# Kernel tuning notes

Hardware: AMD Instinct MI355X
Metric: run time of the kernel (lower is better)

The kernel has to match this reference:

```python
import jax, jax.numpy as jnp
import numpy as np

B, S, E, H = 8, 2048, 1024, 4
D = E // H  # per-head attention embed_dim (torch MHA with num_heads=1)


def setup_inputs() -> dict:
    key = jax.random.key(0)
    ks = jax.random.split(key, 7)
    scale = 0.02
    return {
        "x": jax.random.normal(ks[0], (B, S, E), dtype=jnp.float32),
        # outer linear: torch Linear(E, E) -> y = x @ W.T + b
        "W_lin": jax.random.normal(ks[1], (E, E), dtype=jnp.float32) * scale,
        "b_lin": jnp.zeros((E,), dtype=jnp.float32),
        # per-head MultiheadAttention params, stacked over H heads
        # in_proj: [3D, D] weight, [3D] bias per head (q,k,v stacked)
        "W_in": jax.random.normal(ks[2], (H, 3 * D, D), dtype=jnp.float32) * scale,
        "b_in": jnp.zeros((H, 3 * D), dtype=jnp.float32),
        # out_proj: [D, D] weight, [D] bias per head
        "W_out": jax.random.normal(ks[3], (H, D, D), dtype=jnp.float32) * scale,
        "b_out": jnp.zeros((H, D), dtype=jnp.float32),
    }


def _forward(x, W_lin, b_lin, W_in, b_in, W_out, b_out):
    # outer projection
    x_proj = jnp.einsum("bse,fe->bsf", x, W_lin) + b_lin          # [B,S,E]
    # torch.chunk(dim=-1) into H contiguous slices of width D == reshape
    xs = x_proj.reshape(B, S, H, D)                                 # [B,S,H,D]
    # per-head in_proj (q,k,v share input; weights stacked as [3D, D])
    qkv = jnp.einsum("bshd,hed->bshe", xs, W_in) + b_in             # [B,S,H,3D]
    q, k, v = jnp.split(qkv, 3, axis=-1)                            # each [B,S,H,D]
    # scaled dot-product attention per head (inner num_heads=1 -> head dim D)
    scores = jnp.einsum("bshd,bthd->bhst", q, k) / jnp.sqrt(jnp.float32(D))
    attn = jax.nn.softmax(scores, axis=-1)                          # [B,H,S,S]
    out = jnp.einsum("bhst,bthd->bshd", attn, v)                    # [B,S,H,D]
    # per-head out_proj
    out = jnp.einsum("bshd,hed->bshe", out, W_out) + b_out          # [B,S,H,D]
    # concat heads back along feature dim
    return out.reshape(B, S, E)


def reference(x, W_lin, b_lin, W_in, b_in, W_out, b_out):
    return _forward(x, W_lin, b_lin, W_in, b_in, W_out, b_out)
```

## Files before the change

kernel.cpp:

```cpp
#include <hip/hip_runtime.h>


typedef unsigned short u16;
typedef short s8v __attribute__((ext_vector_type(8)));
typedef float f4v __attribute__((ext_vector_type(4)));
typedef unsigned short us8v __attribute__((ext_vector_type(8)));

typedef const __attribute__((address_space(1))) void* gas_t;
typedef __attribute__((address_space(3))) void* las_t;

#define QSCALE 0.09016844f

__device__ __forceinline__ u16 f2bf(float f) {
  unsigned u = __builtin_bit_cast(unsigned, f);
  unsigned r = u + 0x7FFFu + ((u >> 16) & 1u);
  return (u16)(r >> 16);
}

__device__ __forceinline__ unsigned cvtpk(float a, float b) {
  unsigned r;
  asm("v_cvt_pk_bf16_f32 %0, %1, %2" : "=v"(r) : "v"(a), "v"(b));
  return r;
}

__device__ __forceinline__ void gload16(const void* g, void* l) {
  __builtin_amdgcn_global_load_lds((gas_t)g, (las_t)l, 16, 0, 0);
}

__global__ void cast_kernel(const float* __restrict__ in, u16* __restrict__ out, int n4) {
  int i = blockIdx.x * blockDim.x + threadIdx.x;
  const int stride = gridDim.x * blockDim.x;
  for (; i < n4; i += stride) {
    const float4 v = reinterpret_cast<const float4*>(in)[i];
    ushort4 o;
    o.x = f2bf(v.x); o.y = f2bf(v.y); o.z = f2bf(v.z); o.w = f2bf(v.w);
    reinterpret_cast<ushort4*>(out)[i] = o;
  }
}

__global__ void cast_win(const float* __restrict__ in, u16* __restrict__ out, int n4) {
  const int i = blockIdx.x * blockDim.x + threadIdx.x;
  if (i >= n4) return;
  const float4 v = reinterpret_cast<const float4*>(in)[i];
  const float sc = (((i >> 6) % 768) < 256) ? QSCALE : 1.0f;
  ushort4 o;
  o.x = f2bf(v.x * sc); o.y = f2bf(v.y * sc); o.z = f2bf(v.z * sc); o.w = f2bf(v.w * sc);
  reinterpret_cast<ushort4*>(out)[i] = o;
}

template <int MODE>
__global__ void __launch_bounds__(256, 2) gemm128(
    const u16* __restrict__ A, const u16* __restrict__ Bw,
    const float* __restrict__ bias,
    u16* __restrict__ outB, float* __restrict__ outF,
    u16* __restrict__ Qo, u16* __restrict__ Ko, u16* __restrict__ Vo)
{
  constexpr int K    = (MODE == 0) ? 1024 : 256;
  constexpr int LDA  = 1024;
  constexpr int LDB  = (MODE == 0) ? 1024 : 256;
  constexpr int SMEM = (MODE == 1) ? 35072 : 32768;

  const int bx = blockIdx.x, ny = blockIdx.y, h = blockIdx.z;
  const int tid = threadIdx.x;
  const int wid = tid >> 6, l = tid & 63;
  const int l15 = l & 15, lg = l >> 4;
  const int wr = wid >> 1, wc = wid & 1;

  __shared__ __align__(16) char smem[SMEM];
  char* Al = smem;
  char* Bl = smem + 16384;

  const u16* Abase = A + (size_t)bx * 128 * LDA + ((MODE == 0) ? 0 : h * 256);
  const size_t bwoff = (MODE == 0) ? 0
                      : ((MODE == 1) ? (size_t)h * 768 * 256 : (size_t)h * 256 * 256);
  const u16* Bbase = Bw + bwoff + (size_t)ny * 128 * LDB;

  f4v acc[4][4];
#pragma unroll
  for (int i = 0; i < 4; ++i)
#pragma unroll
    for (int j = 0; j < 4; ++j) acc[i][j] = f4v{0.f, 0.f, 0.f, 0.f};

  for (int k0 = 0; k0 < K; k0 += 64) {
    __syncthreads();
#pragma unroll
    for (int ii = 0; ii < 4; ++ii) {
      const int i = wid * 4 + ii;
      const int row = i * 8 + (l >> 3);
      const int c = l & 7;
      gload16(Abase + (size_t)row * LDA + k0 + ((c ^ (row & 7)) << 3), Al + i * 1024);
    }
#pragma unroll
    for (int ii = 0; ii < 4; ++ii) {
      const int i = wid * 4 + ii;
      const int row = i * 8 + (l >> 3);
      const int c = l & 7;
      gload16(Bbase + (size_t)row * LDB + k0 + ((c ^ (row & 7)) << 3), Bl + i * 1024);
    }
    __syncthreads();
#pragma unroll
    for (int kf = 0; kf < 2; ++kf) {
      s8v a[4];
#pragma unroll
      for (int mf = 0; mf < 4; ++mf) {
        const int row = wr * 64 + mf * 16 + l15;
        a[mf] = *reinterpret_cast<const s8v*>(
            Al + row * 128 + (((kf * 32 + lg * 8) << 1) ^ ((row & 7) << 4)));
      }
#pragma unroll
      for (int nf = 0; nf < 4; ++nf) {
        const int n = wc * 64 + nf * 16 + l15;
        const s8v b = *reinterpret_cast<const s8v*>(
            Bl + n * 128 + (((kf * 32 + lg * 8) << 1) ^ ((n & 7) << 4)));
#pragma unroll
        for (int mf = 0; mf < 4; ++mf)
          acc[mf][nf] = __builtin_amdgcn_mfma_f32_16x16x32_bf16(a[mf], b, acc[mf][nf], 0, 0, 0);
      }
    }
  }

  const int mbase = bx * 128 + wr * 64;
  const int nbase = ny * 128 + wc * 64;

  if constexpr (MODE == 0) {
#pragma unroll
    for (int nf = 0; nf < 4; ++nf) {
      const int colg = nbase + nf * 16 + l15;
      const float bv = bias[colg];
#pragma unroll
      for (int mf = 0; mf < 4; ++mf)
#pragma unroll
        for (int r = 0; r < 4; ++r) {
          const int mr = mbase + mf * 16 + lg * 4 + r;
          outB[(size_t)mr * 1024 + colg] = f2bf(acc[mf][nf][r] + bv);
        }
    }
  } else if constexpr (MODE == 2) {
#pragma unroll
    for (int nf = 0; nf < 4; ++nf) {
      const int colg = nbase + nf * 16 + l15;
      const float bv = bias[h * 256 + colg];
#pragma unroll
      for (int mf = 0; mf < 4; ++mf)
#pragma unroll
        for (int r = 0; r < 4; ++r) {
          const int mr = mbase + mf * 16 + lg * 4 + r;
          outF[(size_t)mr * 1024 + h * 256 + colg] = acc[mf][nf][r] + bv;
        }
    }
  } else {
    if (ny < 4) {
      u16* dst = (ny < 2) ? Qo : Ko;
      const int cb = (ny < 2) ? 0 : 256;
      const float bscale = (ny < 2) ? QSCALE : 1.0f;
#pragma unroll
      for (int nf = 0; nf < 4; ++nf) {
        const int colg = nbase + nf * 16 + l15;
        const float bv = bias[h * 768 + colg] * bscale;
        const int d = colg - cb;
#pragma unroll
        for (int mf = 0; mf < 4; ++mf)
#pragma unroll
          for (int r = 0; r < 4; ++r) {
            const int mr = mbase + mf * 16 + lg * 4 + r;
            const int b = mr >> 11, s = mr & 2047;
            dst[((size_t)(b * 4 + h) * 2048 + s) * 256 + d] = f2bf(acc[mf][nf][r] + bv);
          }
      }
    } else {
      __syncthreads();
      short* tr = reinterpret_cast<short*>(smem);
#pragma unroll
      for (int nf = 0; nf < 4; ++nf) {
        const int colg = nbase + nf * 16 + l15;
        const float bv = bias[h * 768 + colg];
        const int cl = wc * 64 + nf * 16 + l15;
#pragma unroll
        for (int mf = 0; mf < 4; ++mf)
#pragma unroll
          for (int r = 0; r < 4; ++r) {
            const int rl = wr * 64 + mf * 16 + lg * 4 + r;
            tr[rl * 137 + cl] = (short)f2bf(acc[mf][nf][r] + bv);
          }
      }
      __syncthreads();
      const int b = bx >> 4;
#pragma unroll
      for (int rep = 0; rep < 8; ++rep) {
        const int u = rep * 256 + tid;
        const int d = u >> 4, sb = u & 15;
        const int dglob = (ny - 4) * 128 + d;
        const int tile = (bx & 15) * 2 + (sb >> 3);
        const int c = sb & 7;
        const int kA = 32 * (c >> 2) + 8 * ((2 * c) & 3) + 4 * ((c >> 1) & 1);
        u16* base = Vo + (((size_t)(b * 4 + h) * 32 + tile) * 256 + dglob) * 64;
        ushort4 lo, hi;
        lo.x = (u16)tr[(sb * 8 + 0) * 137 + d];
        lo.y = (u16)tr[(sb * 8 + 1) * 137 + d];
        lo.z = (u16)tr[(sb * 8 + 2) * 137 + d];
        lo.w = (u16)tr[(sb * 8 + 3) * 137 + d];
        hi.x = (u16)tr[(sb * 8 + 4) * 137 + d];
        hi.y = (u16)tr[(sb * 8 + 5) * 137 + d];
        hi.z = (u16)tr[(sb * 8 + 6) * 137 + d];
        hi.w = (u16)tr[(sb * 8 + 7) * 137 + d];
        *reinterpret_cast<ushort4*>(base + kA)     = lo;
        *reinterpret_cast<ushort4*>(base + kA + 8) = hi;
      }
    }
  }
}

__global__ void __launch_bounds__(256, 2) attn_fwd(
    const u16* __restrict__ Q, const u16* __restrict__ Kk,
    const u16* __restrict__ Vt, u16* __restrict__ AO)
{
  const int qt = blockIdx.x;
  const int bh = blockIdx.y;
  const int tid = threadIdx.x;
  const int wid = tid >> 6, l = tid & 63;
  const int l15 = l & 15, lg = l >> 4;

  __shared__ __align__(16) char smem[65536];
  char* Kl = smem;
  char* Vl = smem + 32768;

  const size_t kbase = (size_t)bh * 2048 * 256;

  s8v qa[8];
  {
    const u16* qrow = Q + ((size_t)bh * 2048 + qt * 64 + wid * 16 + l15) * 256;
#pragma unroll
    for (int kf = 0; kf < 8; ++kf)
      qa[kf] = *reinterpret_cast<const s8v*>(qrow + kf * 32 + lg * 8);
  }

  f4v O[16];
#pragma unroll
  for (int df = 0; df < 16; ++df) O[df] = f4v{0.f, 0.f, 0.f, 0.f};
  float m_run = -1e30f, l_run = 0.f;

  for (int t0 = 0; t0 < 2048; t0 += 64) {
    __syncthreads();
#pragma unroll
    for (int ii = 0; ii < 8; ++ii) {
      const int i = wid * 8 + ii;
      const int row = i * 2 + (l >> 5);
      const int c = l & 31;
      gload16(Kk + kbase + (size_t)(t0 + row) * 256 + ((c ^ (row & 7)) << 3), Kl + i * 1024);
    }
    {
      const u16* vtile = Vt + ((size_t)bh * 32 + (t0 >> 6)) * 16384;
#pragma unroll
      for (int ii = 0; ii < 8; ++ii) {
        const int i = wid * 8 + ii;
        const int d = i * 8 + (l >> 3);
        const int c = l & 7;
        gload16(vtile + (size_t)d * 64 + ((c ^ (d & 7)) << 3), Vl + i * 1024);
      }
    }
    __syncthreads();

    f4v Sx[4];
#pragma unroll
    for (int nf = 0; nf < 4; ++nf) Sx[nf] = f4v{0.f, 0.f, 0.f, 0.f};
#pragma unroll
    for (int kf = 0; kf < 8; ++kf) {
      const int ch = kf * 4 + lg;
#pragma unroll
      for (int nf = 0; nf < 4; ++nf) {
        const int tl = nf * 16 + l15;
        const s8v kb = *reinterpret_cast<const s8v*>(
            Kl + tl * 512 + ((ch ^ (tl & 7)) << 4));
        Sx[nf] = __builtin_amdgcn_mfma_f32_16x16x32_bf16(kb, qa[kf], Sx[nf], 0, 0, 0);
      }
    }

    float mloc = -1e30f;
#pragma unroll
    for (int nf = 0; nf < 4; ++nf)
#pragma unroll
      for (int r = 0; r < 4; ++r) mloc = fmaxf(mloc, Sx[nf][r]);
    mloc = fmaxf(mloc, __shfl_xor(mloc, 16));
    mloc = fmaxf(mloc, __shfl_xor(mloc, 32));

    if (__any(mloc > m_run + 11.5f)) {
      const float mn = fmaxf(m_run, mloc);
      const float fac = __builtin_exp2f(m_run - mn);
      m_run = mn;
      l_run *= fac;
      float facr[4];
#pragma unroll
      for (int r = 0; r < 4; ++r) facr[r] = __shfl(fac, lg * 4 + r);
#pragma unroll
      for (int df = 0; df < 16; ++df) {
        O[df][0] *= facr[0]; O[df][1] *= facr[1];
        O[df][2] *= facr[2]; O[df][3] *= facr[3];
      }
    }

    float p[4][4];
    float sum = 0.f;
#pragma unroll
    for (int nf = 0; nf < 4; ++nf)
#pragma unroll
      for (int r = 0; r < 4; ++r) {
        p[nf][r] = __builtin_exp2f(Sx[nf][r] - m_run);
        sum += p[nf][r];
      }
    sum += __shfl_xor(sum, 16);
    sum += __shfl_xor(sum, 32);
    l_run += sum;

    s8v pa[2];
#pragma unroll
    for (int kf2 = 0; kf2 < 2; ++kf2) {
      int4 w;
      w.x = (int)cvtpk(p[2 * kf2][0],     p[2 * kf2][1]);
      w.y = (int)cvtpk(p[2 * kf2][2],     p[2 * kf2][3]);
      w.z = (int)cvtpk(p[2 * kf2 + 1][0], p[2 * kf2 + 1][1]);
      w.w = (int)cvtpk(p[2 * kf2 + 1][2], p[2 * kf2 + 1][3]);
      pa[kf2] = __builtin_bit_cast(s8v, w);
    }

#pragma unroll
    for (int kf2 = 0; kf2 < 2; ++kf2) {
      const int ch = kf2 * 4 + lg;
#pragma unroll
      for (int df = 0; df < 16; ++df) {
        const int dl = df * 16 + l15;
        const s8v vb = *reinterpret_cast<const s8v*>(
            Vl + dl * 128 + ((ch ^ (dl & 7)) << 4));
        O[df] = __builtin_amdgcn_mfma_f32_16x16x32_bf16(pa[kf2], vb, O[df], 0, 0, 0);
      }
    }
  }

  const float inv = 1.0f / l_run;
  float invr[4];
#pragma unroll
  for (int r = 0; r < 4; ++r) invr[r] = __shfl(inv, lg * 4 + r);
  const int b = bh >> 2, h = bh & 3;
#pragma unroll
  for (int df = 0; df < 16; ++df)
#pragma unroll
    for (int r = 0; r < 4; ++r) {
      const int srow = qt * 64 + wid * 16 + lg * 4 + r;
      AO[(size_t)(b * 2048 + srow) * 1024 + h * 256 + df * 16 + l15] =
          f2bf(O[df][r] * invr[r]);
    }
}

extern "C" void kernel_launch(void* const* d_in, const int* in_sizes, int n_in,
                              void* d_out, int out_size, void* d_ws, size_t ws_size,
                              hipStream_t stream) {
  (void)in_sizes; (void)n_in; (void)out_size; (void)ws_size;
  const float* x     = (const float*)d_in[0];
  const float* W_lin = (const float*)d_in[1];
  const float* b_lin = (const float*)d_in[2];
  const float* W_in  = (const float*)d_in[3];
  const float* b_in  = (const float*)d_in[4];
  const float* W_out = (const float*)d_in[5];
  const float* b_out = (const float*)d_in[6];

  char* ws = (char*)d_ws;
  u16* Qb  = (u16*)(ws);
  u16* Vtb = (u16*)(ws + (32ull << 20));
  u16* AOb = (u16*)(ws + (64ull << 20));
  u16* WLb = (u16*)(ws + (96ull << 20));
  u16* WIb = (u16*)(ws + (98ull << 20));
  u16* WOb = (u16*)(ws + (98ull << 20) + 1572864ull);

  char* doc  = (char*)d_out;
  u16* xb    = (u16*)doc;
  u16* xproj = (u16*)(doc + (32ull << 20));
  u16* Kb    = (u16*)doc;
  float* outF = (float*)d_out;

  cast_kernel<<<2048, 256, 0, stream>>>(x, xb, 4194304);
  cast_kernel<<<1024, 256, 0, stream>>>(W_lin, WLb, 262144);
  cast_win<<<768, 256, 0, stream>>>(W_in, WIb, 196608);
  cast_kernel<<<256, 256, 0, stream>>>(W_out, WOb, 65536);

  gemm128<0><<<dim3(128, 8, 1), 256, 0, stream>>>(xb, WLb, b_lin, xproj, nullptr,
                                                  nullptr, nullptr, nullptr);
  gemm128<1><<<dim3(128, 6, 4), 256, 0, stream>>>(xproj, WIb, b_in, nullptr, nullptr,
                                                  Qb, Kb, Vtb);
  attn_fwd<<<dim3(32, 32, 1), 256, 0, stream>>>(Qb, Kb, Vtb, AOb);
  gemm128<2><<<dim3(128, 2, 4), 256, 0, stream>>>(AOb, WOb, b_out, nullptr, outF,
                                                  nullptr, nullptr, nullptr);
}
```

Baseline: 330.3 us.

## Process two 16-row query fragments per wave in attention kernel

Each wave now handles 32 query rows (two MFMA M-fragments) instead of 16, so every K and V fragment read from LDS feeds two MFMAs, and each block covers 128 query rows. The grid is halved to 16 query tiles, which halves the number of times each K/V tile is loaded from global memory. The cost is roughly double the accumulator and Q register footprint (O grows to 2x16 f4v), which risks spills or lower occupancy under launch_bounds(256,2), and there are fewer blocks (512) to spread across the CUs.

```diff
diff --git a/kernel.cpp b/kernel.cpp
--- a/kernel.cpp
+++ b/kernel.cpp
@@ -226,18 +226,21 @@
 
   const size_t kbase = (size_t)bh * 2048 * 256;
 
-  s8v qa[8];
-  {
-    const u16* qrow = Q + ((size_t)bh * 2048 + qt * 64 + wid * 16 + l15) * 256;
+  s8v qa[2][8];
+#pragma unroll
+  for (int mf = 0; mf < 2; ++mf) {
+    const u16* qrow = Q + ((size_t)bh * 2048 + qt * 128 + wid * 32 + mf * 16 + l15) * 256;
 #pragma unroll
     for (int kf = 0; kf < 8; ++kf)
-      qa[kf] = *reinterpret_cast<const s8v*>(qrow + kf * 32 + lg * 8);
-  }
-
-  f4v O[16];
-#pragma unroll
-  for (int df = 0; df < 16; ++df) O[df] = f4v{0.f, 0.f, 0.f, 0.f};
-  float m_run = -1e30f, l_run = 0.f;
+      qa[mf][kf] = *reinterpret_cast<const s8v*>(qrow + kf * 32 + lg * 8);
+  }
+
+  f4v O[2][16];
+#pragma unroll
+  for (int mf = 0; mf < 2; ++mf)
+#pragma unroll
+    for (int df = 0; df < 16; ++df) O[mf][df] = f4v{0.f, 0.f, 0.f, 0.f};
+  float m_run[2] = {-1e30f, -1e30f}, l_run[2] = {0.f, 0.f};
 
   for (int t0 = 0; t0 < 2048; t0 += 64) {
     __syncthreads();
@@ -260,9 +263,11 @@
     }
     __syncthreads();
 
-    f4v Sx[4];
-#pragma unroll
-    for (int nf = 0; nf < 4; ++nf) Sx[nf] = f4v{0.f, 0.f, 0.f, 0.f};
+    f4v Sx[2][4];
+#pragma unroll
+    for (int mf = 0; mf < 2; ++mf)
+#pragma unroll
+      for (int nf = 0; nf < 4; ++nf) Sx[mf][nf] = f4v{0.f, 0.f, 0.f, 0.f};
 #pragma unroll
     for (int kf = 0; kf < 8; ++kf) {
       const int ch = kf * 4 + lg;
@@ -271,55 +276,59 @@
         const int tl = nf * 16 + l15;
         const s8v kb = *reinterpret_cast<const s8v*>(
             Kl + tl * 512 + ((ch ^ (tl & 7)) << 4));
-        Sx[nf] = __builtin_amdgcn_mfma_f32_16x16x32_bf16(kb, qa[kf], Sx[nf], 0, 0, 0);
-      }
-    }
-
-    float mloc = -1e30f;
-#pragma unroll
-    for (int nf = 0; nf < 4; ++nf)
-#pragma unroll
-      for (int r = 0; r < 4; ++r) mloc = fmaxf(mloc, Sx[nf][r]);
-    mloc = fmaxf(mloc, __shfl_xor(mloc, 16));
-    mloc = fmaxf(mloc, __shfl_xor(mloc, 32));
-
-    if (__any(mloc > m_run + 11.5f)) {
-      const float mn = fmaxf(m_run, mloc);
-      const float fac = __builtin_exp2f(m_run - mn);
-      m_run = mn;
-      l_run *= fac;
-      float facr[4];
-#pragma unroll
-      for (int r = 0; r < 4; ++r) facr[r] = __shfl(fac, lg * 4 + r);
-#pragma unroll
-      for (int df = 0; df < 16; ++df) {
-        O[df][0] *= facr[0]; O[df][1] *= facr[1];
-        O[df][2] *= facr[2]; O[df][3] *= facr[3];
-      }
-    }
-
-    float p[4][4];
-    float sum = 0.f;
-#pragma unroll
-    for (int nf = 0; nf < 4; ++nf)
-#pragma unroll
-      for (int r = 0; r < 4; ++r) {
-        p[nf][r] = __builtin_exp2f(Sx[nf][r] - m_run);
-        sum += p[nf][r];
-      }
-    sum += __shfl_xor(sum, 16);
-    sum += __shfl_xor(sum, 32);
-    l_run += sum;
-
-    s8v pa[2];
-#pragma unroll
-    for (int kf2 = 0; kf2 < 2; ++kf2) {
-      int4 w;
-      w.x = (int)cvtpk(p[2 * kf2][0],     p[2 * kf2][1]);
-      w.y = (int)cvtpk(p[2 * kf2][2],     p[2 * kf2][3]);
-      w.z = (int)cvtpk(p[2 * kf2 + 1][0], p[2 * kf2 + 1][1]);
-      w.w = (int)cvtpk(p[2 * kf2 + 1][2], p[2 * kf2 + 1][3]);
-      pa[kf2] = __builtin_bit_cast(s8v, w);
+        Sx[0][nf] = __builtin_amdgcn_mfma_f32_16x16x32_bf16(kb, qa[0][kf], Sx[0][nf], 0, 0, 0);
+        Sx[1][nf] = __builtin_amdgcn_mfma_f32_16x16x32_bf16(kb, qa[1][kf], Sx[1][nf], 0, 0, 0);
+      }
+    }
+
+    float p[2][4][4];
+    s8v pa[2][2];
+#pragma unroll
+    for (int mf = 0; mf < 2; ++mf) {
+      float mloc = -1e30f;
+#pragma unroll
+      for (int nf = 0; nf < 4; ++nf)
+#pragma unroll
+        for (int r = 0; r < 4; ++r) mloc = fmaxf(mloc, Sx[mf][nf][r]);
+      mloc = fmaxf(mloc, __shfl_xor(mloc, 16));
+      mloc = fmaxf(mloc, __shfl_xor(mloc, 32));
+
+      if (__any(mloc > m_run[mf] + 11.5f)) {
+        const float mn = fmaxf(m_run[mf], mloc);
+        const float fac = __builtin_exp2f(m_run[mf] - mn);
+        m_run[mf] = mn;
+        l_run[mf] *= fac;
+        float facr[4];
+#pragma unroll
+        for (int r = 0; r < 4; ++r) facr[r] = __shfl(fac, lg * 4 + r);
+#pragma unroll
+        for (int df = 0; df < 16; ++df) {
+          O[mf][df][0] *= facr[0]; O[mf][df][1] *= facr[1];
+          O[mf][df][2] *= facr[2]; O[mf][df][3] *= facr[3];
+        }
+      }
+
+      float sum = 0.f;
+#pragma unroll
+      for (int nf = 0; nf < 4; ++nf)
+#pragma unroll
+        for (int r = 0; r < 4; ++r) {
+          p[mf][nf][r] = __builtin_exp2f(Sx[mf][nf][r] - m_run[mf]);
+          sum += p[mf][nf][r];
+        }
+      sum += __shfl_xor(sum, 16);
+      sum += __shfl_xor(sum, 32);
+      l_run[mf] += sum;
+
+#pragma unroll
+      for (int kf2 = 0; kf2 < 2; ++kf2) {
+        int4 w;
+        w.x = (int)cvtpk(p[mf][2 * kf2][0],     p[mf][2 * kf2][1]);
+        w.y = (int)cvtpk(p[mf][2 * kf2][2],     p[mf][2 * kf2][3]);
+        w.z = (int)cvtpk(p[mf][2 * kf2 + 1][0], p[mf][2 * kf2 + 1][1]);
+        w.w = (int)cvtpk(p[mf][2 * kf2 + 1][2], p[mf][2 * kf2 + 1][3]);
+        pa[mf][kf2] = __builtin_bit_cast(s8v, w);
+      }
     }
 
 #pragma unroll
@@ -330,24 +339,28 @@
         const int dl = df * 16 + l15;
         const s8v vb = *reinterpret_cast<const s8v*>(
             Vl + dl * 128 + ((ch ^ (dl & 7)) << 4));
-        O[df] = __builtin_amdgcn_mfma_f32_16x16x32_bf16(pa[kf2], vb, O[df], 0, 0, 0);
-      }
-    }
-  }
-
-  const float inv = 1.0f / l_run;
-  float invr[4];
-#pragma unroll
-  for (int r = 0; r < 4; ++r) invr[r] = __shfl(inv, lg * 4 + r);
+        O[0][df] = __builtin_amdgcn_mfma_f32_16x16x32_bf16(pa[0][kf2], vb, O[0][df], 0, 0, 0);
+        O[1][df] = __builtin_amdgcn_mfma_f32_16x16x32_bf16(pa[1][kf2], vb, O[1][df], 0, 0, 0);
+      }
+    }
+  }
+
   const int b = bh >> 2, h = bh & 3;
 #pragma unroll
-  for (int df = 0; df < 16; ++df)
-#pragma unroll
-    for (int r = 0; r < 4; ++r) {
-      const int srow = qt * 64 + wid * 16 + lg * 4 + r;
-      AO[(size_t)(b * 2048 + srow) * 1024 + h * 256 + df * 16 + l15] =
-          f2bf(O[df][r] * invr[r]);
-    }
+  for (int mf = 0; mf < 2; ++mf) {
+    const float inv = 1.0f / l_run[mf];
+    float invr[4];
+#pragma unroll
+    for (int r = 0; r < 4; ++r) invr[r] = __shfl(inv, lg * 4 + r);
+#pragma unroll
+    for (int df = 0; df < 16; ++df)
+#pragma unroll
+      for (int r = 0; r < 4; ++r) {
+        const int srow = qt * 128 + wid * 32 + mf * 16 + lg * 4 + r;
+        AO[(size_t)(b * 2048 + srow) * 1024 + h * 256 + df * 16 + l15] =
+            f2bf(O[mf][df][r] * invr[r]);
+      }
+  }
 }
 
 extern "C" void kernel_launch(void* const* d_in, const int* in_sizes, int n_in,
@@ -385,7 +398,7 @@
                                                   nullptr, nullptr, nullptr);
   gemm128<1><<<dim3(128, 6, 4), 256, 0, stream>>>(xproj, WIb, b_in, nullptr, nullptr,
                                                   Qb, Kb, Vtb);
-  attn_fwd<<<dim3(32, 32, 1), 256, 0, stream>>>(Qb, Kb, Vtb, AOb);
+  attn_fwd<<<dim3(16, 32, 1), 256, 0, stream>>>(Qb, Kb, Vtb, AOb);
   gemm128<2><<<dim3(128, 2, 4), 256, 0, stream>>>(AOb, WOb, b_out, nullptr, outF,
                                                   nullptr, nullptr, nullptr);
 }
```

Result: slower. 403.3 us (+22.1%).

## Double-buffer K/V tiles in attention with 32-key tiles and async prefetch

Applied to the files above, without the earlier changes.

The attention kernel now uses 32-key tiles instead of 64 and double-buffers K and V in shared memory. The next tile's global-to-LDS loads are issued before the current tile is computed, and explicit vmcnt waits with barriers replace the two syncthreads per iteration. The V-transpose producer is changed to write 32-wide tiles so they match the new layout. This is meant to hide global load latency behind MFMA work, at the cost of twice as many loop iterations, more barriers, and more frequent online-softmax rescale checks.

```diff
diff --git a/kernel.cpp b/kernel.cpp
--- a/kernel.cpp
+++ b/kernel.cpp
@@ -190,10 +190,10 @@
         const int u = rep * 256 + tid;
         const int d = u >> 4, sb = u & 15;
         const int dglob = (ny - 4) * 128 + d;
-        const int tile = (bx & 15) * 2 + (sb >> 3);
-        const int c = sb & 7;
-        const int kA = 32 * (c >> 2) + 8 * ((2 * c) & 3) + 4 * ((c >> 1) & 1);
-        u16* base = Vo + (((size_t)(b * 4 + h) * 32 + tile) * 256 + dglob) * 64;
+        const int tileg = (bx & 15) * 4 + (sb >> 2);
+        const int c = sb & 3;
+        const int kA = 16 * (c & 1) + 4 * (c >> 1);
+        u16* base = Vo + (((size_t)(b * 4 + h) * 64 + tileg) * 256 + dglob) * 32;
         ushort4 lo, hi;
         lo.x = (u16)tr[(sb * 8 + 0) * 137 + d];
         lo.y = (u16)tr[(sb * 8 + 1) * 137 + d];
@@ -221,8 +221,6 @@
   const int l15 = l & 15, lg = l >> 4;
 
   __shared__ __align__(16) char smem[65536];
-  char* Kl = smem;
-  char* Vl = smem + 32768;
 
   const size_t kbase = (size_t)bh * 2048 * 256;
 
@@ -239,35 +237,52 @@
   for (int df = 0; df < 16; ++df) O[df] = f4v{0.f, 0.f, 0.f, 0.f};
   float m_run = -1e30f, l_run = 0.f;
 
-  for (int t0 = 0; t0 < 2048; t0 += 64) {
-    __syncthreads();
-#pragma unroll
-    for (int ii = 0; ii < 8; ++ii) {
-      const int i = wid * 8 + ii;
+  auto stage = [&](int t, int buf) {
+    const int t0 = t * 32;
+#pragma unroll
+    for (int ii = 0; ii < 4; ++ii) {
+      const int i = wid * 4 + ii;
       const int row = i * 2 + (l >> 5);
       const int c = l & 31;
-      gload16(Kk + kbase + (size_t)(t0 + row) * 256 + ((c ^ (row & 7)) << 3), Kl + i * 1024);
-    }
-    {
-      const u16* vtile = Vt + ((size_t)bh * 32 + (t0 >> 6)) * 16384;
-#pragma unroll
-      for (int ii = 0; ii < 8; ++ii) {
-        const int i = wid * 8 + ii;
-        const int d = i * 8 + (l >> 3);
-        const int c = l & 7;
-        gload16(vtile + (size_t)d * 64 + ((c ^ (d & 7)) << 3), Vl + i * 1024);
-      }
-    }
-    __syncthreads();
-
-    f4v Sx[4];
-#pragma unroll
-    for (int nf = 0; nf < 4; ++nf) Sx[nf] = f4v{0.f, 0.f, 0.f, 0.f};
+      gload16(Kk + kbase + (size_t)(t0 + row) * 256 + ((c ^ (row & 7)) << 3),
+              smem + buf * 16384 + i * 1024);
+    }
+    const u16* vtile = Vt + ((size_t)bh * 64 + t) * 8192;
+#pragma unroll
+    for (int ii = 0; ii < 4; ++ii) {
+      const int i = wid * 4 + ii;
+      const int d = i * 16 + (l >> 2);
+      const int c = l & 3;
+      gload16(vtile + (size_t)d * 32 + ((c ^ (d & 3)) << 3),
+              smem + 32768 + buf * 16384 + i * 1024);
+    }
+  };
+
+  stage(0, 0);
+
+  for (int t = 0; t < 64; ++t) {
+    const int cur = t & 1;
+    if (t < 63) {
+      stage(t + 1, cur ^ 1);
+      asm volatile("s_waitcnt vmcnt(8)" ::: "memory");
+    } else {
+      asm volatile("s_waitcnt vmcnt(0)" ::: "memory");
+    }
+    __builtin_amdgcn_sched_barrier(0);
+    __builtin_amdgcn_s_barrier();
+    __builtin_amdgcn_sched_barrier(0);
+
+    const char* Kl = smem + cur * 16384;
+    const char* Vl = smem + 32768 + cur * 16384;
+
+    f4v Sx[2];
+    Sx[0] = f4v{0.f, 0.f, 0.f, 0.f};
+    Sx[1] = f4v{0.f, 0.f, 0.f, 0.f};
 #pragma unroll
     for (int kf = 0; kf < 8; ++kf) {
       const int ch = kf * 4 + lg;
 #pragma unroll
-      for (int nf = 0; nf < 4; ++nf) {
+      for (int nf = 0; nf < 2; ++nf) {
         const int tl = nf * 16 + l15;
         const s8v kb = *reinterpret_cast<const s8v*>(
             Kl + tl * 512 + ((ch ^ (tl & 7)) << 4));
@@ -275,11 +290,8 @@
       }
     }
 
-    float mloc = -1e30f;
-#pragma unroll
-    for (int nf = 0; nf < 4; ++nf)
-#pragma unroll
-      for (int r = 0; r < 4; ++r) mloc = fmaxf(mloc, Sx[nf][r]);
+    float mloc = fmaxf(fmaxf(fmaxf(Sx[0][0], Sx[0][1]), fmaxf(Sx[0][2], Sx[0][3])),
+                       fmaxf(fmaxf(Sx[1][0], Sx[1][1]), fmaxf(Sx[1][2], Sx[1][3])));
     mloc = fmaxf(mloc, __shfl_xor(mloc, 16));
     mloc = fmaxf(mloc, __shfl_xor(mloc, 32));
 
@@ -298,10 +310,10 @@
       }
     }
 
-    float p[4][4];
+    float p[2][4];
     float sum = 0.f;
 #pragma unroll
-    for (int nf = 0; nf < 4; ++nf)
+    for (int nf = 0; nf < 2; ++nf)
 #pragma unroll
       for (int r = 0; r < 4; ++r) {
         p[nf][r] = __builtin_exp2f(Sx[nf][r] - m_run);
@@ -311,28 +323,27 @@
     sum += __shfl_xor(sum, 32);
     l_run += sum;
 
-    s8v pa[2];
-#pragma unroll
-    for (int kf2 = 0; kf2 < 2; ++kf2) {
+    s8v pa;
+    {
       int4 w;
-      w.x = (int)cvtpk(p[2 * kf2][0],     p[2 * kf2][1]);
-      w.y = (int)cvtpk(p[2 * kf2][2],     p[2 * kf2][3]);
-      w.z = (int)cvtpk(p[2 * kf2 + 1][0], p[2 * kf2 + 1][1]);
-      w.w = (int)cvtpk(p[2 * kf2 + 1][2], p[2 * kf2 + 1][3]);
-      pa[kf2] = __builtin_bit_cast(s8v, w);
-    }
-
-#pragma unroll
-    for (int kf2 = 0; kf2 < 2; ++kf2) {
-      const int ch = kf2 * 4 + lg;
-#pragma unroll
-      for (int df = 0; df < 16; ++df) {
-        const int dl = df * 16 + l15;
-        const s8v vb = *reinterpret_cast<const s8v*>(
-            Vl + dl * 128 + ((ch ^ (dl & 7)) << 4));
-        O[df] = __builtin_amdgcn_mfma_f32_16x16x32_bf16(pa[kf2], vb, O[df], 0, 0, 0);
-      }
-    }
+      w.x = (int)cvtpk(p[0][0], p[0][1]);
+      w.y = (int)cvtpk(p[0][2], p[0][3]);
+      w.z = (int)cvtpk(p[1][0], p[1][1]);
+      w.w = (int)cvtpk(p[1][2], p[1][3]);
+      pa = __builtin_bit_cast(s8v, w);
+    }
+
+#pragma unroll
+    for (int df = 0; df < 16; ++df) {
+      const int dl = df * 16 + l15;
+      const s8v vb = *reinterpret_cast<const s8v*>(
+          Vl + dl * 64 + ((lg ^ (dl & 3)) << 4));
+      O[df] = __builtin_amdgcn_mfma_f32_16x16x32_bf16(pa, vb, O[df], 0, 0, 0);
+    }
+
+    __builtin_amdgcn_sched_barrier(0);
+    __builtin_amdgcn_s_barrier();
+    __builtin_amdgcn_sched_barrier(0);
   }
 
   const float inv = 1.0f / l_run;
```

Measured after the change: 362.3 us. 1.1x slower.

## Switch attention to 32x32x16 MFMA with 2-wave blocks and new V layout

Applied to the files above, without the earlier changes.

Rewrites the attention kernel to use 32x32x16 bf16 MFMA instead of 16x16x32, with 128-thread blocks where each wave owns 32 query rows. The V tile layout written by the QKV GEMM epilogue and the K/V shared-memory swizzles change to match the new operand fragments. The lazy rescale branch is dropped in favour of an unconditional rescale, and the row sum is taken over the bf16-rounded probabilities. Larger MFMA tiles mean fewer LDS reads per flop, but the kernel now runs half as many waves per block at one block per CU by launch bounds, which may cut latency hiding. The 64 KB of shared memory per block is unchanged.

```diff
diff --git a/kernel.cpp b/kernel.cpp
--- a/kernel.cpp
+++ b/kernel.cpp
@@ -4,6 +4,7 @@
 typedef unsigned short u16;
 typedef short s8v __attribute__((ext_vector_type(8)));
 typedef float f4v __attribute__((ext_vector_type(4)));
+typedef float f16v __attribute__((ext_vector_type(16)));
 typedef unsigned short us8v __attribute__((ext_vector_type(8)));
 
 typedef const __attribute__((address_space(1))) void* gas_t;
@@ -188,29 +189,32 @@
 #pragma unroll
       for (int rep = 0; rep < 8; ++rep) {
         const int u = rep * 256 + tid;
-        const int d = u >> 4, sb = u & 15;
-        const int dglob = (ny - 4) * 128 + d;
+        const int dloc = u >> 4;
+        const int sb = u & 15;
+        const int dglob = (ny - 4) * 128 + dloc;
         const int tile = (bx & 15) * 2 + (sb >> 3);
-        const int c = sb & 7;
-        const int kA = 32 * (c >> 2) + 8 * ((2 * c) & 3) + 4 * ((c >> 1) & 1);
-        u16* base = Vo + (((size_t)(b * 4 + h) * 32 + tile) * 256 + dglob) * 64;
-        ushort4 lo, hi;
-        lo.x = (u16)tr[(sb * 8 + 0) * 137 + d];
-        lo.y = (u16)tr[(sb * 8 + 1) * 137 + d];
-        lo.z = (u16)tr[(sb * 8 + 2) * 137 + d];
-        lo.w = (u16)tr[(sb * 8 + 3) * 137 + d];
-        hi.x = (u16)tr[(sb * 8 + 4) * 137 + d];
-        hi.y = (u16)tr[(sb * 8 + 5) * 137 + d];
-        hi.z = (u16)tr[(sb * 8 + 6) * 137 + d];
-        hi.w = (u16)tr[(sb * 8 + 7) * 137 + d];
-        *reinterpret_cast<ushort4*>(base + kA)     = lo;
-        *reinterpret_cast<ushort4*>(base + kA + 8) = hi;
+        const int kvg = (sb >> 1) & 3;
+        const int r = dglob >> 1;
+        const int c0 = (dglob & 1) * 8 + kvg * 2;
+        const int j0 = (sb & 1) * 4;
+        u16* tb = Vo + ((size_t)(b * 4 + h) * 32 + tile) * 16384;
+        ushort4 lo, hv;
+        lo.x = (u16)tr[(sb * 8 + 0) * 137 + dloc];
+        lo.y = (u16)tr[(sb * 8 + 1) * 137 + dloc];
+        lo.z = (u16)tr[(sb * 8 + 2) * 137 + dloc];
+        lo.w = (u16)tr[(sb * 8 + 3) * 137 + dloc];
+        hv.x = (u16)tr[(sb * 8 + 4) * 137 + dloc];
+        hv.y = (u16)tr[(sb * 8 + 5) * 137 + dloc];
+        hv.z = (u16)tr[(sb * 8 + 6) * 137 + dloc];
+        hv.w = (u16)tr[(sb * 8 + 7) * 137 + dloc];
+        *reinterpret_cast<ushort4*>(tb + r * 128 + ((c0 ^ (r & 15)) << 3) + j0) = lo;
+        *reinterpret_cast<ushort4*>(tb + r * 128 + (((c0 + 1) ^ (r & 15)) << 3) + j0) = hv;
       }
     }
   }
 }
 
-__global__ void __launch_bounds__(256, 2) attn_fwd(
+__global__ void __launch_bounds__(128, 1) attn_fwd(
     const u16* __restrict__ Q, const u16* __restrict__ Kk,
     const u16* __restrict__ Vt, u16* __restrict__ AO)
 {
@@ -218,7 +222,7 @@
   const int bh = blockIdx.y;
   const int tid = threadIdx.x;
   const int wid = tid >> 6, l = tid & 63;
-  const int l15 = l & 15, lg = l >> 4;
+  const int l31 = l & 31, hi = l >> 5;
 
   __shared__ __align__(16) char smem[65536];
   char* Kl = smem;
@@ -226,127 +230,134 @@
 
   const size_t kbase = (size_t)bh * 2048 * 256;
 
-  s8v qa[8];
+  s8v qb[16];
   {
-    const u16* qrow = Q + ((size_t)bh * 2048 + qt * 64 + wid * 16 + l15) * 256;
-#pragma unroll
-    for (int kf = 0; kf < 8; ++kf)
-      qa[kf] = *reinterpret_cast<const s8v*>(qrow + kf * 32 + lg * 8);
+    const u16* qrow = Q + ((size_t)bh * 2048 + qt * 64 + wid * 32 + l31) * 256;
+#pragma unroll
+    for (int step = 0; step < 16; ++step)
+      qb[step] = *reinterpret_cast<const s8v*>(qrow + step * 16 + hi * 8);
   }
 
-  f4v O[16];
-#pragma unroll
-  for (int df = 0; df < 16; ++df) O[df] = f4v{0.f, 0.f, 0.f, 0.f};
+  f16v O[8];
+#pragma unroll
+  for (int g = 0; g < 8; ++g)
+#pragma unroll
+    for (int r = 0; r < 16; ++r) O[g][r] = 0.f;
   float m_run = -1e30f, l_run = 0.f;
 
-  for (int t0 = 0; t0 < 2048; t0 += 64) {
+  for (int t = 0; t < 32; ++t) {
     __syncthreads();
 #pragma unroll
-    for (int ii = 0; ii < 8; ++ii) {
-      const int i = wid * 8 + ii;
-      const int row = i * 2 + (l >> 5);
-      const int c = l & 31;
-      gload16(Kk + kbase + (size_t)(t0 + row) * 256 + ((c ^ (row & 7)) << 3), Kl + i * 1024);
+    for (int ii = 0; ii < 16; ++ii) {
+      const int id = ii * 128 + tid;
+      const int kv = id >> 5, c = id & 31;
+      gload16(Kk + kbase + (size_t)(t * 64 + kv) * 256 + ((c ^ (kv & 15)) << 3),
+              Kl + id * 16);
     }
     {
-      const u16* vtile = Vt + ((size_t)bh * 32 + (t0 >> 6)) * 16384;
-#pragma unroll
-      for (int ii = 0; ii < 8; ++ii) {
-        const int i = wid * 8 + ii;
-        const int d = i * 8 + (l >> 3);
-        const int c = l & 7;
-        gload16(vtile + (size_t)d * 64 + ((c ^ (d & 7)) << 3), Vl + i * 1024);
+      const u16* vtile = Vt + ((size_t)bh * 32 + t) * 16384;
+#pragma unroll
+      for (int ii = 0; ii < 16; ++ii) {
+        const int id = ii * 128 + tid;
+        gload16(vtile + id * 8, Vl + id * 16);
       }
     }
     __syncthreads();
 
-    f4v Sx[4];
-#pragma unroll
-    for (int nf = 0; nf < 4; ++nf) Sx[nf] = f4v{0.f, 0.f, 0.f, 0.f};
-#pragma unroll
-    for (int kf = 0; kf < 8; ++kf) {
-      const int ch = kf * 4 + lg;
-#pragma unroll
-      for (int nf = 0; nf < 4; ++nf) {
-        const int tl = nf * 16 + l15;
-        const s8v kb = *reinterpret_cast<const s8v*>(
-            Kl + tl * 512 + ((ch ^ (tl & 7)) << 4));
-        Sx[nf] = __builtin_amdgcn_mfma_f32_16x16x32_bf16(kb, qa[kf], Sx[nf], 0, 0, 0);
-      }
+    f16v Sx0, Sx1;
+#pragma unroll
+    for (int r = 0; r < 16; ++r) { Sx0[r] = 0.f; Sx1[r] = 0.f; }
+#pragma unroll
+    for (int step = 0; step < 16; ++step) {
+      const int coff = ((step * 2 + hi) ^ (l & 15)) << 4;
+      const s8v kb0 = *reinterpret_cast<const s8v*>(Kl + l31 * 512 + coff);
+      const s8v kb1 = *reinterpret_cast<const s8v*>(Kl + (32 + l31) * 512 + coff);
+      Sx0 = __builtin_amdgcn_mfma_f32_32x32x16_bf16(kb0, qb[step], Sx0, 0, 0, 0);
+      Sx1 = __builtin_amdgcn_mfma_f32_32x32x16_bf16(kb1, qb[step], Sx1, 0, 0, 0);
     }
 
     float mloc = -1e30f;
 #pragma unroll
-    for (int nf = 0; nf < 4; ++nf)
-#pragma unroll
-      for (int r = 0; r < 4; ++r) mloc = fmaxf(mloc, Sx[nf][r]);
-    mloc = fmaxf(mloc, __shfl_xor(mloc, 16));
+    for (int r = 0; r < 16; ++r) mloc = fmaxf(mloc, fmaxf(Sx0[r], Sx1[r]));
     mloc = fmaxf(mloc, __shfl_xor(mloc, 32));
 
-    if (__any(mloc > m_run + 11.5f)) {
-      const float mn = fmaxf(m_run, mloc);
-      const float fac = __builtin_exp2f(m_run - mn);
-      m_run = mn;
-      l_run *= fac;
-      float facr[4];
-#pragma unroll
-      for (int r = 0; r < 4; ++r) facr[r] = __shfl(fac, lg * 4 + r);
-#pragma unroll
-      for (int df = 0; df < 16; ++df) {
-        O[df][0] *= facr[0]; O[df][1] *= facr[1];
-        O[df][2] *= facr[2]; O[df][3] *= facr[3];
-      }
-    }
-
-    float p[4][4];
+    const float mn = fmaxf(m_run, mloc);
+    const float fac = __builtin_exp2f(m_run - mn);
+    m_run = mn;
+    l_run *= fac;
+    {
+      float facr[16];
+#pragma unroll
+      for (int r = 0; r < 16; ++r)
+        facr[r] = __shfl(fac, (r & 3) + 8 * (r >> 2) + 4 * hi);
+#pragma unroll
+      for (int g = 0; g < 8; ++g)
+#pragma unroll
+        for (int r = 0; r < 16; ++r) O[g][r] *= facr[r];
+    }
+
+#pragma unroll
+    for (int r = 0; r < 16; ++r) {
+      Sx0[r] = __builtin_exp2f(Sx0[r] - mn);
+      Sx1[r] = __builtin_exp2f(Sx1[r] - mn);
+    }
+
+    unsigned w[16];
+    w[0]  = cvtpk(Sx0[0],  Sx0[1]);  w[1]  = cvtpk(Sx0[2],  Sx0[3]);
+    w[2]  = cvtpk(Sx0[4],  Sx0[5]);  w[3]  = cvtpk(Sx0[6],  Sx0[7]);
+    w[4]  = cvtpk(Sx0[8],  Sx0[9]);  w[5]  = cvtpk(Sx0[10], Sx0[11]);
+    w[6]  = cvtpk(Sx0[12], Sx0[13]); w[7]  = cvtpk(Sx0[14], Sx0[15]);
+    w[8]  = cvtpk(Sx1[0],  Sx1[1]);  w[9]  = cvtpk(Sx1[2],  Sx1[3]);
+    w[10] = cvtpk(Sx1[4],  Sx1[5]);  w[11] = cvtpk(Sx1[6],  Sx1[7]);
+    w[12] = cvtpk(Sx1[8],  Sx1[9]);  w[13] = cvtpk(Sx1[10], Sx1[11]);
+    w[14] = cvtpk(Sx1[12], Sx1[13]); w[15] = cvtpk(Sx1[14], Sx1[15]);
+
     float sum = 0.f;
 #pragma unroll
-    for (int nf = 0; nf < 4; ++nf)
-#pragma unroll
-      for (int r = 0; r < 4; ++r) {
-        p[nf][r] = __builtin_exp2f(Sx[nf][r] - m_run);
-        sum += p[nf][r];
-      }
-    sum += __shfl_xor(sum, 16);
+    for (int i = 0; i < 16; ++i)
+      sum += __builtin_bit_cast(float, w[i] << 16) +
+             __builtin_bit_cast(float, w[i] & 0xFFFF0000u);
     sum += __shfl_xor(sum, 32);
     l_run += sum;
 
-    s8v pa[2];
-#pragma unroll
-    for (int kf2 = 0; kf2 < 2; ++kf2) {
-      int4 w;
-      w.x = (int)cvtpk(p[2 * kf2][0],     p[2 * kf2][1]);
-      w.y = (int)cvtpk(p[2 * kf2][2],     p[2 * kf2][3]);
-      w.z = (int)cvtpk(p[2 * kf2 + 1][0], p[2 * kf2 + 1][1]);
-      w.w = (int)cvtpk(p[2 * kf2 + 1][2], p[2 * kf2 + 1][3]);
-      pa[kf2] = __builtin_bit_cast(s8v, w);
-    }
-
-#pragma unroll
-    for (int kf2 = 0; kf2 < 2; ++kf2) {
-      const int ch = kf2 * 4 + lg;
-#pragma unroll
-      for (int df = 0; df < 16; ++df) {
-        const int dl = df * 16 + l15;
+    s8v pa[4];
+    {
+      int4 w0 = {(int)w[0],  (int)w[1],  (int)w[2],  (int)w[3]};
+      int4 w1 = {(int)w[4],  (int)w[5],  (int)w[6],  (int)w[7]};
+      int4 w2 = {(int)w[8],  (int)w[9],  (int)w[10], (int)w[11]};
+      int4 w3 = {(int)w[12], (int)w[13], (int)w[14], (int)w[15]};
+      pa[0] = __builtin_bit_cast(s8v, w0);
+      pa[1] = __builtin_bit_cast(s8v, w1);
+      pa[2] = __builtin_bit_cast(s8v, w2);
+      pa[3] = __builtin_bit_cast(s8v, w3);
+    }
+
+#pragma unroll
+    for (int kvg = 0; kvg < 4; ++kvg) {
+#pragma unroll
+      for (int Mg = 0; Mg < 8; ++Mg) {
+        const int rr = Mg * 16 + (l31 >> 1);
+        const int c = (l & 1) * 8 + kvg * 2 + hi;
         const s8v vb = *reinterpret_cast<const s8v*>(
-            Vl + dl * 128 + ((ch ^ (dl & 7)) << 4));
-        O[df] = __builtin_amdgcn_mfma_f32_16x16x32_bf16(pa[kf2], vb, O[df], 0, 0, 0);
+            Vl + rr * 256 + ((c ^ (rr & 15)) << 4));
+        O[Mg] = __builtin_amdgcn_mfma_f32_32x32x16_bf16(pa[kvg], vb, O[Mg], 0, 0, 0);
       }
     }
   }
 
   const float inv = 1.0f / l_run;
-  float invr[4];
-#pragma unroll
-  for (int r = 0; r < 4; ++r) invr[r] = __shfl(inv, lg * 4 + r);
+  float invr[16];
+#pragma unroll
+  for (int r = 0; r < 16; ++r)
+    invr[r] = __shfl(inv, (r & 3) + 8 * (r >> 2) + 4 * hi);
   const int b = bh >> 2, h = bh & 3;
 #pragma unroll
-  for (int df = 0; df < 16; ++df)
-#pragma unroll
-    for (int r = 0; r < 4; ++r) {
-      const int srow = qt * 64 + wid * 16 + lg * 4 + r;
-      AO[(size_t)(b * 2048 + srow) * 1024 + h * 256 + df * 16 + l15] =
-          f2bf(O[df][r] * invr[r]);
+  for (int Mg = 0; Mg < 8; ++Mg)
+#pragma unroll
+    for (int r = 0; r < 16; ++r) {
+      const int srow = qt * 64 + wid * 32 + (r & 3) + 8 * (r >> 2) + 4 * hi;
+      AO[(size_t)(b * 2048 + srow) * 1024 + h * 256 + Mg * 32 + l31] =
+          f2bf(O[Mg][r] * invr[r]);
     }
 }
 
@@ -385,7 +396,7 @@
                                                   nullptr, nullptr, nullptr);
   gemm128<1><<<dim3(128, 6, 4), 256, 0, stream>>>(xproj, WIb, b_in, nullptr, nullptr,
                                                   Qb, Kb, Vtb);
-  attn_fwd<<<dim3(32, 32, 1), 256, 0, stream>>>(Qb, Kb, Vtb, AOb);
+  attn_fwd<<<dim3(32, 32, 1), 128, 0, stream>>>(Qb, Kb, Vtb, AOb);
   gemm128<2><<<dim3(128, 2, 4), 256, 0, stream>>>(AOb, WOb, b_out, nullptr, outF,
                                                   nullptr, nullptr, nullptr);
 }
```

After: 397.8 us. 20.4% more time.
